# Kernel optimization log

Measured on AMD Instinct MI355X. Metric: run time of the kernel, lower is better.

Reference implementation:

```python
import jax, jax.numpy as jnp
import numpy as np

TWO_PI = 2.0 * np.pi
ALPHA = 0.65
KSIZE = (3, 3, 3)   # (kOr, kH, kW)
ITERS = 1
BN_EPS = 1e-5


def _interp(v, dy, dx):
    """Bilinear sample of v[b,c,o, y+dy[o], x+dx[o]], border-clamped.
    v: [B,C,Or,H,W]; dy, dx: [Or] float per-orientation constant shifts."""
    H, W = v.shape[3], v.shape[4]
    y0 = jnp.floor(dy); fy = dy - y0; y0 = y0.astype(jnp.int32)
    iy = jnp.arange(H)[None, :] + y0[:, None]                      # [Or,H]
    g0 = jnp.take_along_axis(v, jnp.clip(iy, 0, H - 1)[None, None, :, :, None], axis=3)
    g1 = jnp.take_along_axis(v, jnp.clip(iy + 1, 0, H - 1)[None, None, :, :, None], axis=3)
    fyb = fy[None, None, :, None, None]
    v = (1.0 - fyb) * g0 + fyb * g1
    x0 = jnp.floor(dx); fx = dx - x0; x0 = x0.astype(jnp.int32)
    ix = jnp.arange(W)[None, :] + x0[:, None]                      # [Or,W]
    h0 = jnp.take_along_axis(v, jnp.clip(ix, 0, W - 1)[None, None, :, None, :], axis=4)
    h1 = jnp.take_along_axis(v, jnp.clip(ix + 1, 0, W - 1)[None, None, :, None, :], axis=4)
    fxb = fx[None, None, :, None, None]
    return (1.0 - fxb) * h0 + fxb * h1


def _convection(u, g0):
    """out[b,c,p] = u[b,c, p . g0[c]^{-1}] via trilinear resampling.
    Sample point: ((x,y) - R(theta - th0)@(x0,y0), theta - th0), theta periodic."""
    Or = u.shape[2]
    def one(uc, g):  # uc: [B,Or,H,W], g = (x0, y0, th0)
        x0, y0, th0 = g[0], g[1], g[2]
        t = th0 * Or / TWO_PI
        i = jnp.floor(t); f = t - i; i = i.astype(jnp.int32)
        # periodic linear interpolation along orientation axis
        v = (1.0 - f) * jnp.roll(uc, i, axis=1) + f * jnp.roll(uc, i + 1, axis=1)
        a = jnp.arange(Or, dtype=u.dtype) * (TWO_PI / Or) - th0
        dx = -(jnp.cos(a) * x0 - jnp.sin(a) * y0)
        dy = -(jnp.sin(a) * x0 + jnp.cos(a) * y0)
        return _interp(v[:, None], dy, dx)[:, 0]
    return jax.vmap(one, in_axes=(1, 0), out_axes=1)(u, g0)


def _se2_log(qx, qy, dth):
    """Exact SE(2) logarithm coordinates (c1,c2,c3) of group offset (qx,qy,dth)."""
    if abs(dth) < 1e-9:
        return qx, qy, dth
    h = 0.5 * dth
    cot = np.cos(h) / np.sin(h)
    return h * (qx * cot + qy), h * (-qx + qy * cot), dth


def _morph(u, metric, dilate):
    """Fractional morphological dilation (max of u(p.q) - k(q)) or erosion
    (min of u(p.q) + k(q)) with left-invariant Riemannian kernel
    k_c(q) = nu_a * d_c(q)^{2a/(2a-1)}, d_c^2 = (m0*c1)^2+(m1*c2)^2+(m2*c3)^2."""
    kOr, kH, kW = KSIZE
    Or = u.shape[2]
    thetas = jnp.arange(Or, dtype=u.dtype) * (TWO_PI / Or)
    p = 2.0 * ALPHA / (2.0 * ALPHA - 1.0)
    nu = (2.0 * ALPHA - 1.0) * (2.0 * ALPHA) ** (-p)
    out = None
    for qt in range(-(kOr // 2), kOr // 2 + 1):
        dth = qt * TWO_PI / Or
        for qy in range(-(kH // 2), kH // 2 + 1):
            for qx in range(-(kW // 2), kW // 2 + 1):
                c1, c2, c3 = _se2_log(float(qx), float(qy), dth)
                s = (metric[:, 0] * c1) ** 2 + (metric[:, 1] * c2) ** 2 + (metric[:, 2] * c3) ** 2
                k = nu * s ** (p / 2.0)                       # [C]
                # left-invariant shift: spatial offset rotated by theta_o
                dxo = jnp.cos(thetas) * qx - jnp.sin(thetas) * qy
                dyo = jnp.sin(thetas) * qx + jnp.cos(thetas) * qy
                val = _interp(jnp.roll(u, -qt, axis=2), dyo, dxo)
                kb = k[None, :, None, None, None]
                cand = val - kb if dilate else val + kb
                if out is None:
                    out = cand
                else:
                    out = jnp.maximum(out, cand) if dilate else jnp.minimum(out, cand)
    return out


def setup_inputs() -> dict:
    key = jax.random.key(0)
    ks = jax.random.split(key, 5)
    B, Cin, Cout, Or, H, W = 4, 8, 16, 8, 128, 128
    x = jax.random.normal(ks[0], (B, Cin, Or, H, W), dtype=jnp.float32)
    g0 = 0.5 * jax.random.normal(ks[1], (Cin, 3), dtype=jnp.float32)
    lo, hi = 1.4 / 3.0, 0.7 * 3.0   # reset_parameters range for metric params
    metric_dil = jax.random.uniform(ks[2], (Cin, 3), minval=lo, maxval=hi, dtype=jnp.float32)
    metric_ero = jax.random.uniform(ks[3], (Cin, 3), minval=lo, maxval=hi, dtype=jnp.float32)
    bound = 0.25  # kaiming_uniform(a=sqrt(5)) bound for [8,16] weight
    weight = jax.random.uniform(ks[4], (Cin, Cout), minval=-bound, maxval=bound, dtype=jnp.float32)
    gamma = jnp.ones((Cout,), jnp.float32)
    beta = jnp.zeros((Cout,), jnp.float32)
    return dict(x=x, g0=g0, metric_dil=metric_dil, metric_ero=metric_ero,
                weight=weight, gamma=gamma, beta=beta)


def reference(x, g0, metric_dil, metric_ero, weight, gamma, beta):
    u = x
    for _ in range(ITERS):
        u = _convection(u, g0)
        u = _morph(u, metric_dil, dilate=True)
        u = _morph(u, metric_ero, dilate=False)
    # channel mixing: [B,Cin,Or,H,W] x [Cin,Cout] -> [B,Cout,Or,H,W]
    y = jnp.einsum('bcohw,cd->bdohw', u, weight)
    # BatchNorm3d (training mode): per-channel stats over (B,Or,H,W)
    m = y.mean(axis=(0, 2, 3, 4), keepdims=True)
    v = y.var(axis=(0, 2, 3, 4), keepdims=True)
    yh = (y - m) * jax.lax.rsqrt(v + BN_EPS)
    return yh * gamma[None, :, None, None, None] + beta[None, :, None, None, None]
```

## Files before the change

kernel.cpp:

```cpp
#include <hip/hip_runtime.h>
#include <math.h>
#include <utility>

#define B 4
#define CIN 8
#define COUT 16
#define OR_ 8
#define H_ 128
#define W_ 128
#define HW 16384
#define PLANE HW
#define CH_STR (OR_*HW)
#define BATCH_STR (CIN*CH_STR)
#define NELEM (B*BATCH_STR)
#define NPOS (B*OR_*HW)
#define NB_RED 512

#define TILE 16
#define CB_DIM 24
#define CB_S   28
#define CB_PL  (CB_DIM*CB_S)
#define DB_DIM 20
#define DB_S   28
#define DB_PL  (DB_DIM*DB_S)

typedef __attribute__((ext_vector_type(4))) float f4;

struct Tables {
  float kdil[CIN][27];
  float kero[CIN][27];
  int   conv_i[CIN];
  float conv_f[CIN];
  float conv_dy[CIN][OR_];
  float conv_dx[CIN][OR_];
};

__host__ __device__ constexpr double m_cos(int o) {
  const double r = 0.70710678118654752440;
  const double t[8] = {1.0, r, 0.0, -r, -1.0, -r, 0.0, r};
  return t[o];
}
__host__ __device__ constexpr double m_sin(int o) {
  const double r = 0.70710678118654752440;
  const double t[8] = {0.0, r, 1.0, r, 0.0, -r, -1.0, -r};
  return t[o];
}
__host__ __device__ constexpr double tap_dx(int o, int j) {
  return m_cos(o)*(j % 3 - 1) - m_sin(o)*(j / 3 - 1);
}
__host__ __device__ constexpr double tap_dy(int o, int j) {
  return m_sin(o)*(j % 3 - 1) + m_cos(o)*(j / 3 - 1);
}
__host__ __device__ constexpr int ifloor(double v) {
  int i = (int)v;
  return ((double)i > v) ? i - 1 : i;
}
__host__ __device__ constexpr int tap_ix(int o, int j) { return ifloor(tap_dx(o, j)); }
__host__ __device__ constexpr int tap_iy(int o, int j) { return ifloor(tap_dy(o, j)); }
__host__ __device__ constexpr float tap_fx(int o, int j) { return (float)(tap_dx(o, j) - tap_ix(o, j)); }
__host__ __device__ constexpr float tap_fy(int o, int j) { return (float)(tap_dy(o, j) - tap_iy(o, j)); }
__host__ __device__ constexpr float corner_w(int o, int j, int dyb, int dxb) {
  float fy = tap_fy(o, j), fx = tap_fx(o, j);
  return (dyb ? fy : 1.0f - fy) * (dxb ? fx : 1.0f - fx);
}
__host__ __device__ constexpr int corner_r(int o, int j, int dyb) { return tap_iy(o, j) + dyb + 2; }
__host__ __device__ constexpr int corner_c(int o, int j, int i, int dxb) { return i + tap_ix(o, j) + dxb + 2; }
__host__ __device__ constexpr bool row_used(int o, int r) {
  for (int j = 0; j < 9; ++j)
    for (int dyb = 0; dyb < 2; ++dyb)
      for (int dxb = 0; dxb < 2; ++dxb)
        if (corner_w(o, j, dyb, dxb) != 0.0f && corner_r(o, j, dyb) == r)
          return true;
  return false;
}

template<int N> struct Rep {
  template<class F> __device__ __forceinline__ static void run(F&& f) {
    Rep<N-1>::run(f);
    f(std::integral_constant<int, N-1>{});
  }
};
template<> struct Rep<0> {
  template<class F> __device__ __forceinline__ static void run(F&&) {}
};


__global__ void precompute_kernel(const float* __restrict__ g0,
                                  const float* __restrict__ mdil,
                                  const float* __restrict__ mero,
                                  Tables* __restrict__ T) {
  const int t = threadIdx.x;
  const double TWO_PI = 6.283185307179586476925286766559;
  const double P  = 2.0*0.65/(2.0*0.65 - 1.0);
  const double NU = (2.0*0.65 - 1.0)*pow(2.0*0.65, -P);
  if (t < 432) {
    int which = t / 216;
    int r = t % 216;
    int c = r / 27;
    int j = r % 27;
    int qt = j/9 - 1;
    int qy = (j/3)%3 - 1;
    int qx = j%3 - 1;
    double dth = qt * (TWO_PI/OR_);
    double c1, c2, c3;
    if (qt == 0) { c1 = qx; c2 = qy; c3 = 0.0; }
    else {
      double h = 0.5*dth;
      double cot = cos(h)/sin(h);
      c1 = h*(qx*cot + qy);
      c2 = h*(-qx + qy*cot);
      c3 = dth;
    }
    const float* m = which ? mero : mdil;
    double a0 = (double)m[c*3+0]*c1;
    double a1 = (double)m[c*3+1]*c2;
    double a2 = (double)m[c*3+2]*c3;
    double s = a0*a0 + a1*a1 + a2*a2;
    float k = (float)(NU * pow(s, P*0.5));
    if (which) T->kero[c][j] = k; else T->kdil[c][j] = k;
  } else if (t >= 512 && t < 512 + CIN*OR_) {
    int r = t - 512;
    int c = r / OR_;
    int o = r % OR_;
    float x0 = g0[c*3+0], y0 = g0[c*3+1], th0 = g0[c*3+2];
    float a = (float)(o*(TWO_PI/OR_)) - th0;
    float ca = cosf(a), sa = sinf(a);
    T->conv_dx[c][o] = -(ca*x0 - sa*y0);
    T->conv_dy[c][o] = -(sa*x0 + ca*y0);
    if (o == 0) {
      float tt = th0 * (float)(OR_/TWO_PI);
      float fi = floorf(tt);
      T->conv_i[c] = (int)fi;
      T->conv_f[c] = tt - fi;
    }
  }
}

template<int O, int DIL, int PLSTR, int RSTR>
__device__ __forceinline__ void morph_tile_lds(const float* __restrict__ src,
                                               const float* __restrict__ kt,
                                               int row, int gc, float acc[4]) {
  Rep<3>::run([&](auto qc) {
    constexpr int qti = decltype(qc)::value;
    const float* p = src + ((O + qti + 7) & 7) * PLSTR + row * RSTR + gc;
    float win[5][8];
    Rep<5>::run([&](auto rc) {
      constexpr int r = decltype(rc)::value;
      if constexpr (row_used(O, r)) {
        f4 lo = *(const f4*)(p + r*RSTR);
        f4 hi = *(const f4*)(p + r*RSTR + 4);
        win[r][0] = lo.x; win[r][1] = lo.y; win[r][2] = lo.z; win[r][3] = lo.w;
        win[r][4] = hi.x; win[r][5] = hi.y; win[r][6] = hi.z; win[r][7] = hi.w;
      }
    });
    Rep<9>::run([&](auto jc) {
      constexpr int j = decltype(jc)::value;
      float k = kt[qti*9 + j];
      float base = DIL ? -k : k;
      Rep<4>::run([&](auto ic) {
        constexpr int i = decltype(ic)::value;
        float v = base;
        Rep<4>::run([&](auto cc2) {
          constexpr int cn  = decltype(cc2)::value;
          constexpr int dyb = cn >> 1, dxb = cn & 1;
          constexpr float Wgt = corner_w(O, j, dyb, dxb);
          if constexpr (Wgt != 0.0f) {
            constexpr int R = corner_r(O, j, dyb);
            constexpr int C = corner_c(O, j, i, dxb);
            v = fmaf(Wgt, win[R][C], v);
          }
        });
        acc[i] = DIL ? fmaxf(acc[i], v) : fminf(acc[i], v);
      });
    });
  });
}

template<int O>
__device__ __forceinline__ void dil_wave(const float* __restrict__ cb, float* __restrict__ db,
                                         const float* __restrict__ kt, int lane) {
  #pragma unroll
  for (int it = 0; it < 2; ++it) {
    int g = lane + it*64;
    if (g < 100) {
      int row = g / 5;
      int gc = (g - row*5) * 4;
      float acc[4] = {-INFINITY, -INFINITY, -INFINITY, -INFINITY};
      morph_tile_lds<O, 1, CB_PL, CB_S>(cb, kt, row, gc, acc);
      f4 v = {acc[0], acc[1], acc[2], acc[3]};
      *(f4*)(db + O*DB_PL + row*DB_S + gc) = v;
    }
  }
}

template<int O>
__device__ __forceinline__ void ero_wave(const float* __restrict__ db, float* __restrict__ dst,
                                         const float* __restrict__ kt, int lane) {
  int row = lane >> 2;
  int gc = (lane & 3) * 4;
  float acc[4] = {INFINITY, INFINITY, INFINITY, INFINITY};
  morph_tile_lds<O, 0, DB_PL, DB_S>(db, kt, row, gc, acc);
  f4 v = {acc[0], acc[1], acc[2], acc[3]};
  *(f4*)(dst + O*PLANE + row*W_ + gc) = v;
}

__global__ __launch_bounds__(512, 4)
void fused_kernel(const float* __restrict__ x, float* __restrict__ u3,
                  const Tables* __restrict__ T) {
  __shared__ float convbuf[8*CB_PL];
  __shared__ float dilbuf[8*DB_PL];
  int blk = blockIdx.x;
  int tx = blk & 7, ty = (blk >> 3) & 7, c = (blk >> 6) & 7, b = blk >> 9;
  int h0 = ty*TILE, w0 = tx*TILE;
  int t = threadIdx.x;
  int wid = t >> 6, lane = t & 63;

  const int   ci = T->conv_i[c];
  const float cf = T->conv_f[c];
  const float* xc = x + b*BATCH_STR + c*CH_STR;
  #pragma unroll
  for (int k = 0; k < 9; ++k) {
    int cc = t + k*512;
    int col = cc % CB_DIM;
    int tmp = cc / CB_DIM;
    int r = tmp % CB_DIM;
    int o = tmp / CB_DIM;
    int gh = min(max(h0 - 4 + r, 0), 127);
    int gw = min(max(w0 - 4 + col, 0), 127);
    int o1 = (o - ci) & 7, o2 = (o - ci - 1) & 7;
    const float* p1 = xc + o1*PLANE;
    const float* p2 = xc + o2*PLANE;
    float dy = T->conv_dy[c][o], dx = T->conv_dx[c][o];
    float fy0 = floorf(dy); float fy = dy - fy0;
    float fx0 = floorf(dx); float fx = dx - fx0;
    int iy = gh + (int)fy0;
    int ix = gw + (int)fx0;
    int r0 = min(max(iy, 0), 127), r1 = min(max(iy+1, 0), 127);
    int c0 = min(max(ix, 0), 127), c1 = min(max(ix+1, 0), 127);
    float w00 = (1.f-fy)*(1.f-fx), w01 = (1.f-fy)*fx, w10 = fy*(1.f-fx), w11 = fy*fx;
    float v1 = w00*p1[r0*W_+c0] + w01*p1[r0*W_+c1] + w10*p1[r1*W_+c0] + w11*p1[r1*W_+c1];
    float v2 = w00*p2[r0*W_+c0] + w01*p2[r0*W_+c1] + w10*p2[r1*W_+c0] + w11*p2[r1*W_+c1];
    convbuf[(o*CB_DIM + r)*CB_S + col] = (1.0f - cf)*v1 + cf*v2;
  }
  __syncthreads();

  {
    const float* kt = T->kdil[c];
    switch (wid) {
      case 0: dil_wave<0>(convbuf, dilbuf, kt, lane); break;
      case 1: dil_wave<1>(convbuf, dilbuf, kt, lane); break;
      case 2: dil_wave<2>(convbuf, dilbuf, kt, lane); break;
      case 3: dil_wave<3>(convbuf, dilbuf, kt, lane); break;
      case 4: dil_wave<4>(convbuf, dilbuf, kt, lane); break;
      case 5: dil_wave<5>(convbuf, dilbuf, kt, lane); break;
      case 6: dil_wave<6>(convbuf, dilbuf, kt, lane); break;
      default: dil_wave<7>(convbuf, dilbuf, kt, lane); break;
    }
  }
  __syncthreads();

  if ((h0 == 0) | (h0 == 112) | (w0 == 0) | (w0 == 112)) {
    #pragma unroll
    for (int k = 0; k < 7; ++k) {
      int cc = t + k*512;
      if (cc < 3200) {
        int col = cc % DB_DIM;
        int tmp = cc / DB_DIM;
        int row = tmp % DB_DIM;
        int o = tmp / DB_DIM;
        int vh = h0 - 2 + row, vw = w0 - 2 + col;
        int dr = min(max(vh, 0), 127) - vh;
        int dc = min(max(vw, 0), 127) - vw;
        if ((dr != 0) | (dc != 0)) {
          dilbuf[(o*DB_DIM + row)*DB_S + col] =
            dilbuf[(o*DB_DIM + row + dr)*DB_S + col + dc];
        }
      }
    }
  }
  __syncthreads();

  {
    const float* kt = T->kero[c];
    float* dst = u3 + (b*CIN + c)*(OR_*PLANE) + h0*W_ + w0;
    switch (wid) {
      case 0: ero_wave<0>(dilbuf, dst, kt, lane); break;
      case 1: ero_wave<1>(dilbuf, dst, kt, lane); break;
      case 2: ero_wave<2>(dilbuf, dst, kt, lane); break;
      case 3: ero_wave<3>(dilbuf, dst, kt, lane); break;
      case 4: ero_wave<4>(dilbuf, dst, kt, lane); break;
      case 5: ero_wave<5>(dilbuf, dst, kt, lane); break;
      case 6: ero_wave<6>(dilbuf, dst, kt, lane); break;
      default: ero_wave<7>(dilbuf, dst, kt, lane); break;
    }
  }
}

__global__ void gram_kernel(const float* __restrict__ u, double* __restrict__ part) {
  int t4 = blockIdx.x*256 + threadIdx.x;
  int hw = (t4 & 4095) << 2;
  int o  = (t4 >> 12) & 7;
  int b  = t4 >> 15;
  const float* base = u + b*BATCH_STR + o*PLANE + hw;
  f4 v[8];
  #pragma unroll
  for (int c = 0; c < 8; c++) v[c] = *(const f4*)(base + c*CH_STR);
  float S[8], G[36];
  #pragma unroll
  for (int c = 0; c < 8; c++) S[c] = v[c].x + v[c].y + v[c].z + v[c].w;
  {
    int t = 0;
    #pragma unroll
    for (int c = 0; c < 8; c++)
      #pragma unroll
      for (int c2 = c; c2 < 8; c2++) {
        G[t] = v[c].x*v[c2].x + v[c].y*v[c2].y + v[c].z*v[c2].z + v[c].w*v[c2].w;
        t++;
      }
  }
  __shared__ double lds[4][44];
  int lane = threadIdx.x & 63;
  int wave = threadIdx.x >> 6;
  for (int t = 0; t < 44; t++) {
    double vv = (double)((t < 8) ? S[t] : G[t-8]);
    for (int off = 32; off; off >>= 1) vv += __shfl_down(vv, off);
    if (lane == 0) lds[wave][t] = vv;
  }
  __syncthreads();
  if (threadIdx.x < 44) {
    part[blockIdx.x*44 + threadIdx.x] =
      lds[0][threadIdx.x] + lds[1][threadIdx.x] + lds[2][threadIdx.x] + lds[3][threadIdx.x];
  }
}

__global__ void stats_kernel(const double* __restrict__ part, const float* __restrict__ weight,
                             const float* __restrict__ gamma, const float* __restrict__ beta,
                             float* __restrict__ ss) {
  __shared__ double tot[44];
  int t = threadIdx.x;
  if (t < 44) {
    double s = 0.0;
    for (int bidx = 0; bidx < NB_RED; bidx++) s += part[bidx*44 + t];
    tot[t] = s;
  }
  __syncthreads();
  if (t < 16) {
    double m = 0.0;
    for (int c = 0; c < 8; c++) m += (double)weight[c*COUT + t] * tot[c];
    double e2 = 0.0;
    int idx = 8;
    for (int c = 0; c < 8; c++)
      for (int c2 = c; c2 < 8; c2++) {
        double wp = (double)weight[c*COUT + t] * (double)weight[c2*COUT + t];
        e2 += (c2 == c ? 1.0 : 2.0) * wp * tot[idx];
        idx++;
      }
    double N = (double)NPOS;
    m /= N; e2 /= N;
    double var = e2 - m*m;
    double inv = rsqrt(var + 1e-5);
    float sc = (float)(inv * (double)gamma[t]);
    ss[t]      = sc;
    ss[16 + t] = beta[t] - (float)m * sc;
  }
}

__global__ void final_kernel(const float* __restrict__ u, const float* __restrict__ weight,
                             const float* __restrict__ ss, float* __restrict__ out) {
  __shared__ float Wsh[8][16];
  __shared__ float scale[16], shift[16];
  int t = threadIdx.x;
  if (t < 128) Wsh[t >> 4][t & 15] = weight[t];
  if (t < 16) { scale[t] = ss[t]; shift[t] = ss[16 + t]; }
  __syncthreads();
  int t4 = blockIdx.x*256 + threadIdx.x;
  int hw = (t4 & 4095) << 2;
  int o  = (t4 >> 12) & 7;
  int b  = t4 >> 15;
  const float* base = u + b*BATCH_STR + o*PLANE + hw;
  f4 v[8];
  #pragma unroll
  for (int c = 0; c < 8; c++) v[c] = *(const f4*)(base + c*CH_STR);
  float* ob = out + b*(COUT*CH_STR) + o*PLANE + hw;
  #pragma unroll
  for (int d = 0; d < 16; d++) {
    f4 y = {0.f, 0.f, 0.f, 0.f};
    #pragma unroll
    for (int c = 0; c < 8; c++) {
      float wv = Wsh[c][d];
      y.x = fmaf(v[c].x, wv, y.x);
      y.y = fmaf(v[c].y, wv, y.y);
      y.z = fmaf(v[c].z, wv, y.z);
      y.w = fmaf(v[c].w, wv, y.w);
    }
    float sc = scale[d], sh = shift[d];
    f4 r = { fmaf(y.x, sc, sh), fmaf(y.y, sc, sh), fmaf(y.z, sc, sh), fmaf(y.w, sc, sh) };
    *(f4*)(ob + d*CH_STR) = r;
  }
}

extern "C" void kernel_launch(void* const* d_in, const int* in_sizes, int n_in,
                              void* d_out, int out_size, void* d_ws, size_t ws_size,
                              hipStream_t stream) {
  const float* x      = (const float*)d_in[0];
  const float* g0     = (const float*)d_in[1];
  const float* mdil   = (const float*)d_in[2];
  const float* mero   = (const float*)d_in[3];
  const float* weight = (const float*)d_in[4];
  const float* gamma  = (const float*)d_in[5];
  const float* beta   = (const float*)d_in[6];
  float* out = (float*)d_out;

  char* ws = (char*)d_ws;
  Tables* T    = (Tables*)ws;
  float*  ss   = (float*)(ws + 8*1024);
  double* part = (double*)(ws + 16*1024);
  float*  u3   = (float*)(ws + (size_t)1*1024*1024);

  precompute_kernel<<<1, 1024, 0, stream>>>(g0, mdil, mero, T);
  fused_kernel<<<B*CIN*64, 512, 0, stream>>>(x, u3, T);
  gram_kernel<<<NB_RED, 256, 0, stream>>>(u3, part);
  stats_kernel<<<1, 64, 0, stream>>>(part, weight, gamma, beta, ss);
  final_kernel<<<NPOS/4/256, 256, 0, stream>>>(u3, weight, ss, out);
}
```

Measured before the change: 119.5 us.

## Precompute convection tables, add interior fast path, pad LDS, widen gram reduction

```diff
diff --git a/kernel.cpp b/kernel.cpp
--- a/kernel.cpp
+++ b/kernel.cpp
@@ -14,14 +14,14 @@
 #define BATCH_STR (CIN*CH_STR)
 #define NELEM (B*BATCH_STR)
 #define NPOS (B*OR_*HW)
-#define NB_RED 512
+#define NB_RED 256
 
 #define TILE 16
 #define CB_DIM 24
-#define CB_S   28
+#define CB_S   29
 #define CB_PL  (CB_DIM*CB_S)
 #define DB_DIM 20
-#define DB_S   28
+#define DB_S   21
 #define DB_PL  (DB_DIM*DB_S)
 
 typedef __attribute__((ext_vector_type(4))) float f4;
@@ -29,10 +29,11 @@
 struct Tables {
   float kdil[CIN][27];
   float kero[CIN][27];
-  int   conv_i[CIN];
-  float conv_f[CIN];
-  float conv_dy[CIN][OR_];
-  float conv_dx[CIN][OR_];
+  int   o1[CIN][OR_], o2[CIN][OR_];
+  int   iy0[CIN][OR_], ix0[CIN][OR_];
+  float w00[CIN][OR_], w01[CIN][OR_], w10[CIN][OR_], w11[CIN][OR_];
+  float cf[CIN];
+  int   iymin[CIN], iymax[CIN], ixmin[CIN], ixmax[CIN];
 };
 
 __host__ __device__ constexpr double m_cos(int o) {
@@ -120,19 +121,37 @@
     if (which) T->kero[c][j] = k; else T->kdil[c][j] = k;
   } else if (t >= 512 && t < 512 + CIN*OR_) {
     int r = t - 512;
-    int c = r / OR_;
-    int o = r % OR_;
+    int c = r >> 3;
+    int o = r & 7;
     float x0 = g0[c*3+0], y0 = g0[c*3+1], th0 = g0[c*3+2];
     float a = (float)(o*(TWO_PI/OR_)) - th0;
     float ca = cosf(a), sa = sinf(a);
-    T->conv_dx[c][o] = -(ca*x0 - sa*y0);
-    T->conv_dy[c][o] = -(sa*x0 + ca*y0);
-    if (o == 0) {
-      float tt = th0 * (float)(OR_/TWO_PI);
-      float fi = floorf(tt);
-      T->conv_i[c] = (int)fi;
-      T->conv_f[c] = tt - fi;
-    }
+    float dxv = -(ca*x0 - sa*y0);
+    float dyv = -(sa*x0 + ca*y0);
+    float fy0 = floorf(dyv), fx0 = floorf(dxv);
+    float fy = dyv - fy0, fx = dxv - fx0;
+    T->iy0[c][o] = (int)fy0;
+    T->ix0[c][o] = (int)fx0;
+    T->w00[c][o] = (1.f-fy)*(1.f-fx);
+    T->w01[c][o] = (1.f-fy)*fx;
+    T->w10[c][o] = fy*(1.f-fx);
+    T->w11[c][o] = fy*fx;
+    float tt = th0 * (float)(OR_/TWO_PI);
+    float fi = floorf(tt);
+    int ci = (int)fi;
+    T->o1[c][o] = (o - ci) & 7;
+    T->o2[c][o] = (o - ci - 1) & 7;
+    if (o == 0) T->cf[c] = tt - fi;
+  }
+  __syncthreads();
+  if (t < CIN) {
+    int iymn = 999, iymx = -999, ixmn = 999, ixmx = -999;
+    for (int o = 0; o < OR_; ++o) {
+      iymn = min(iymn, T->iy0[t][o]); iymx = max(iymx, T->iy0[t][o]);
+      ixmn = min(ixmn, T->ix0[t][o]); ixmx = max(ixmx, T->ix0[t][o]);
+    }
+    T->iymin[t] = iymn; T->iymax[t] = iymx;
+    T->ixmin[t] = ixmn; T->ixmax[t] = ixmx;
   }
 }
 
@@ -147,10 +166,8 @@
     Rep<5>::run([&](auto rc) {
       constexpr int r = decltype(rc)::value;
       if constexpr (row_used(O, r)) {
-        f4 lo = *(const f4*)(p + r*RSTR);
-        f4 hi = *(const f4*)(p + r*RSTR + 4);
-        win[r][0] = lo.x; win[r][1] = lo.y; win[r][2] = lo.z; win[r][3] = lo.w;
-        win[r][4] = hi.x; win[r][5] = hi.y; win[r][6] = hi.z; win[r][7] = hi.w;
+        #pragma unroll
+        for (int k = 0; k < 8; ++k) win[r][k] = p[r*RSTR + k];
       }
     });
     Rep<9>::run([&](auto jc) {
@@ -187,8 +204,9 @@
       int gc = (g - row*5) * 4;
       float acc[4] = {-INFINITY, -INFINITY, -INFINITY, -INFINITY};
       morph_tile_lds<O, 1, CB_PL, CB_S>(cb, kt, row, gc, acc);
-      f4 v = {acc[0], acc[1], acc[2], acc[3]};
-      *(f4*)(db + O*DB_PL + row*DB_S + gc) = v;
+      float* d = db + O*DB_PL + row*DB_S + gc;
+      #pragma unroll
+      for (int i = 0; i < 4; ++i) d[i] = acc[i];
     }
   }
 }
@@ -214,33 +232,60 @@
   int h0 = ty*TILE, w0 = tx*TILE;
   int t = threadIdx.x;
   int wid = t >> 6, lane = t & 63;
-
-  const int   ci = T->conv_i[c];
-  const float cf = T->conv_f[c];
   const float* xc = x + b*BATCH_STR + c*CH_STR;
-  #pragma unroll
-  for (int k = 0; k < 9; ++k) {
-    int cc = t + k*512;
-    int col = cc % CB_DIM;
-    int tmp = cc / CB_DIM;
-    int r = tmp % CB_DIM;
-    int o = tmp / CB_DIM;
-    int gh = min(max(h0 - 4 + r, 0), 127);
-    int gw = min(max(w0 - 4 + col, 0), 127);
-    int o1 = (o - ci) & 7, o2 = (o - ci - 1) & 7;
-    const float* p1 = xc + o1*PLANE;
-    const float* p2 = xc + o2*PLANE;
-    float dy = T->conv_dy[c][o], dx = T->conv_dx[c][o];
-    float fy0 = floorf(dy); float fy = dy - fy0;
-    float fx0 = floorf(dx); float fx = dx - fx0;
-    int iy = gh + (int)fy0;
-    int ix = gw + (int)fx0;
-    int r0 = min(max(iy, 0), 127), r1 = min(max(iy+1, 0), 127);
-    int c0 = min(max(ix, 0), 127), c1 = min(max(ix+1, 0), 127);
-    float w00 = (1.f-fy)*(1.f-fx), w01 = (1.f-fy)*fx, w10 = fy*(1.f-fx), w11 = fy*fx;
-    float v1 = w00*p1[r0*W_+c0] + w01*p1[r0*W_+c1] + w10*p1[r1*W_+c0] + w11*p1[r1*W_+c1];
-    float v2 = w00*p2[r0*W_+c0] + w01*p2[r0*W_+c1] + w10*p2[r1*W_+c0] + w11*p2[r1*W_+c1];
-    convbuf[(o*CB_DIM + r)*CB_S + col] = (1.0f - cf)*v1 + cf*v2;
+
+  {
+    const int o = wid;
+    const int iy0 = T->iy0[c][o], ix0 = T->ix0[c][o];
+    const float w00 = T->w00[c][o], w01 = T->w01[c][o];
+    const float w10 = T->w10[c][o], w11 = T->w11[c][o];
+    const float cfv = T->cf[c];
+    const float* p1 = xc + T->o1[c][o]*PLANE;
+    const float* p2 = xc + T->o2[c][o]*PLANE;
+    bool interior = (h0 - 4 + T->iymin[c] >= 0) & (h0 + 20 + T->iymax[c] <= 127)
+                  & (w0 - 4 + T->ixmin[c] >= 0) & (w0 + 20 + T->ixmax[c] <= 127)
+                  & (h0 >= 16) & (h0 <= 96) & (w0 >= 16) & (w0 <= 96);
+    if (interior) {
+      #pragma unroll
+      for (int it = 0; it < 3; ++it) {
+        int q = lane + it*64;
+        if (q < 144) {
+          int r = q / 6;
+          int cq = q - r*6;
+          int iy = h0 - 4 + r + iy0;
+          int ix = w0 - 4 + cq*4 + ix0;
+          const float* q1 = p1 + iy*W_ + ix;
+          const float* q2 = p2 + iy*W_ + ix;
+          float a[5], bb[5], cc[5], dd[5];
+          #pragma unroll
+          for (int k = 0; k < 5; ++k) {
+            a[k] = q1[k]; bb[k] = q1[W_+k]; cc[k] = q2[k]; dd[k] = q2[W_+k];
+          }
+          float* dst = &convbuf[o*CB_PL + r*CB_S + cq*4];
+          #pragma unroll
+          for (int i = 0; i < 4; ++i) {
+            float v1 = w00*a[i] + w01*a[i+1] + w10*bb[i] + w11*bb[i+1];
+            float v2 = w00*cc[i] + w01*cc[i+1] + w10*dd[i] + w11*dd[i+1];
+            dst[i] = (1.0f - cfv)*v1 + cfv*v2;
+          }
+        }
+      }
+    } else {
+      #pragma unroll
+      for (int it = 0; it < 9; ++it) {
+        int cell = lane + it*64;
+        int r = cell / 24;
+        int col = cell - r*24;
+        int gh = min(max(h0 - 4 + r, 0), 127);
+        int gw = min(max(w0 - 4 + col, 0), 127);
+        int iy = gh + iy0, ix = gw + ix0;
+        int r0 = min(max(iy, 0), 127), r1 = min(max(iy+1, 0), 127);
+        int c0 = min(max(ix, 0), 127), c1 = min(max(ix+1, 0), 127);
+        float v1 = w00*p1[r0*W_+c0] + w01*p1[r0*W_+c1] + w10*p1[r1*W_+c0] + w11*p1[r1*W_+c1];
+        float v2 = w00*p2[r0*W_+c0] + w01*p2[r0*W_+c1] + w10*p2[r1*W_+c0] + w11*p2[r1*W_+c1];
+        convbuf[o*CB_PL + r*CB_S + col] = (1.0f - cfv)*v1 + cfv*v2;
+      }
+    }
   }
   __syncthreads();
 
@@ -272,8 +317,28 @@
         int dr = min(max(vh, 0), 127) - vh;
         int dc = min(max(vw, 0), 127) - vw;
         if ((dr != 0) | (dc != 0)) {
-          dilbuf[(o*DB_DIM + row)*DB_S + col] =
-            dilbuf[(o*DB_DIM + row + dr)*DB_S + col + dc];
+          dilbuf[o*DB_PL + (row + dr)*DB_S + col + dc] ==
+          dilbuf[o*DB_PL + row*DB_S + col];
+        }
+      }
+    }
+  }
+  __syncthreads();
+  if ((h0 == 0) | (h0 == 112) | (w0 == 0) | (w0 == 112)) {
+    #pragma unroll
+    for (int k = 0; k < 7; ++k) {
+      int cc = t + k*512;
+      if (cc < 3200) {
+        int col = cc % DB_DIM;
+        int tmp = cc / DB_DIM;
+        int row = tmp % DB_DIM;
+        int o = tmp / DB_DIM;
+        int vh = h0 - 2 + row, vw = w0 - 2 + col;
+        int dr = min(max(vh, 0), 127) - vh;
+        int dc = min(max(vw, 0), 127) - vw;
+        if ((dr != 0) | (dc != 0)) {
+          dilbuf[o*DB_PL + row*DB_S + col] =
+            dilbuf[o*DB_PL + (row + dr)*DB_S + col + dc];
         }
       }
     }
@@ -297,24 +362,30 @@
 }
 
 __global__ void gram_kernel(const float* __restrict__ u, double* __restrict__ part) {
-  int t4 = blockIdx.x*256 + threadIdx.x;
-  int hw = (t4 & 4095) << 2;
-  int o  = (t4 >> 12) & 7;
-  int b  = t4 >> 15;
+  int t8 = blockIdx.x*256 + threadIdx.x;
+  int hw = (t8 & 2047) << 3;
+  int o  = (t8 >> 11) & 7;
+  int b  = t8 >> 14;
   const float* base = u + b*BATCH_STR + o*PLANE + hw;
-  f4 v[8];
+  f4 v0[8], v1[8];
   #pragma unroll
-  for (int c = 0; c < 8; c++) v[c] = *(const f4*)(base + c*CH_STR);
+  for (int c = 0; c < 8; c++) {
+    v0[c] = *(const f4*)(base + c*CH_STR);
+    v1[c] = *(const f4*)(base + c*CH_STR + 4);
+  }
   float S[8], G[36];
   #pragma unroll
-  for (int c = 0; c < 8; c++) S[c] = v[c].x + v[c].y + v[c].z + v[c].w;
+  for (int c = 0; c < 8; c++)
+    S[c] = (v0[c].x + v0[c].y) + (v0[c].z + v0[c].w)
+         + (v1[c].x + v1[c].y) + (v1[c].z + v1[c].w);
   {
     int t = 0;
     #pragma unroll
     for (int c = 0; c < 8; c++)
       #pragma unroll
       for (int c2 = c; c2 < 8; c2++) {
-        G[t] = v[c].x*v[c2].x + v[c].y*v[c2].y + v[c].z*v[c2].z + v[c].w*v[c2].w;
+        G[t] = v0[c].x*v0[c2].x + v0[c].y*v0[c2].y + v0[c].z*v0[c2].z + v0[c].w*v0[c2].w
+             + v1[c].x*v1[c2].x + v1[c].y*v1[c2].y + v1[c].z*v1[c2].z + v1[c].w*v1[c2].w;
         t++;
       }
   }
@@ -338,10 +409,15 @@
                              float* __restrict__ ss) {
   __shared__ double tot[44];
   int t = threadIdx.x;
-  if (t < 44) {
+  if (t < 352) {
+    int cnt = t >> 3, j = t & 7;
     double s = 0.0;
-    for (int bidx = 0; bidx < NB_RED; bidx++) s += part[bidx*44 + t];
-    tot[t] = s;
+    #pragma unroll 8
+    for (int k = 0; k < 32; ++k) s += part[(j + (k << 3))*44 + cnt];
+    s += __shfl_down(s, 4);
+    s += __shfl_down(s, 2);
+    s += __shfl_down(s, 1);
+    if (j == 0) tot[cnt] = s;
   }
   __syncthreads();
   if (t < 16) {
@@ -420,6 +496,6 @@
   precompute_kernel<<<1, 1024, 0, stream>>>(g0, mdil, mero, T);
   fused_kernel<<<B*CIN*64, 512, 0, stream>>>(x, u3, T);
   gram_kernel<<<NB_RED, 256, 0, stream>>>(u3, part);
-  stats_kernel<<<1, 64, 0, stream>>>(part, weight, gamma, beta, ss);
+  stats_kernel<<<1, 384, 0, stream>>>(part, weight, gamma, beta, ss);
   final_kernel<<<NPOS/4/256, 256, 0, stream>>>(u3, weight, ss, out);
 }
```

After: 116.8 us. -2.3%, faster.
